# Optimization experiments

Hardware: AMD Instinct MI355X
Metric: run time of the kernel (lower is better)

## Reference

```python
import jax, jax.numpy as jnp
import numpy as np

EMBED_DIM = 1024
NUM_HEADS = 16
HEAD_DIM = EMBED_DIM // NUM_HEADS
NUM_GLOBAL = 2
NUM_RANDOM = 3
WINDOW_SIZE = 3
B, S = 2, 2048


def setup_inputs() -> dict:
    key = jax.random.key(0)
    ks = jax.random.split(key, 10)
    scale = 0.02
    inp = {
        "x": jax.random.normal(ks[0], (B, S, EMBED_DIM), dtype=jnp.float32),
        "random_indices": jax.random.randint(ks[1], (S, NUM_RANDOM), 0, S, dtype=jnp.int32),
        "q_w": jax.random.normal(ks[2], (EMBED_DIM, EMBED_DIM), dtype=jnp.float32) * scale,
        "q_b": jnp.zeros((EMBED_DIM,), dtype=jnp.float32),
        "k_w": jax.random.normal(ks[3], (EMBED_DIM, EMBED_DIM), dtype=jnp.float32) * scale,
        "k_b": jnp.zeros((EMBED_DIM,), dtype=jnp.float32),
        "v_w": jax.random.normal(ks[4], (EMBED_DIM, EMBED_DIM), dtype=jnp.float32) * scale,
        "v_b": jnp.zeros((EMBED_DIM,), dtype=jnp.float32),
        "o_w": jax.random.normal(ks[5], (EMBED_DIM, EMBED_DIM), dtype=jnp.float32) * scale,
        "o_b": jnp.zeros((EMBED_DIM,), dtype=jnp.float32),
    }
    return inp


def _build_mask(random_indices, seq_len):
    # [S, S] boolean BigBird mask: global rows/cols + sliding window + random.
    i = jnp.arange(seq_len)[:, None]
    j = jnp.arange(seq_len)[None, :]
    glob = (i < NUM_GLOBAL) | (j < NUM_GLOBAL)
    win = jnp.abs(i - j) <= WINDOW_SIZE
    rand = jnp.zeros((seq_len, seq_len), dtype=bool)
    rows = jnp.repeat(jnp.arange(seq_len), NUM_RANDOM)
    rand = rand.at[rows, random_indices.reshape(-1)].set(True)
    return glob | win | rand


def reference(x, random_indices, q_w, q_b, k_w, k_b, v_w, v_b, o_w, o_b):
    b, s, _ = x.shape
    # torch nn.Linear: y = x @ W.T + b
    q = (x @ q_w.T + q_b).reshape(b, s, NUM_HEADS, HEAD_DIM).transpose(0, 2, 1, 3)
    k = (x @ k_w.T + k_b).reshape(b, s, NUM_HEADS, HEAD_DIM).transpose(0, 2, 1, 3)
    v = (x @ v_w.T + v_b).reshape(b, s, NUM_HEADS, HEAD_DIM).transpose(0, 2, 1, 3)
    scores = jnp.einsum("bhqd,bhkd->bhqk", q, k) / jnp.sqrt(jnp.float32(HEAD_DIM))
    mask = _build_mask(random_indices, s)  # [S, S]
    scores = jnp.where(mask[None, None, :, :], scores, -jnp.inf)
    probs = jax.nn.softmax(scores, axis=-1)
    out = jnp.einsum("bhqk,bhkd->bhqd", probs, v)
    out = out.transpose(0, 2, 1, 3).reshape(b, s, EMBED_DIM)
    return out @ o_w.T + o_b
```

## Files before the change

kernel.cpp:

```cpp
#include <hip/hip_runtime.h>

#define B_  2
#define S_  2048
#define E_  1024
#define H_  16
#define D_  64
#define NGLOB 2
#define NRAND 3
#define WIN 3

typedef __bf16 bf16x8 __attribute__((ext_vector_type(8)));
typedef float  f32x4  __attribute__((ext_vector_type(4)));

__device__ __forceinline__ unsigned short f2bf(float f) {
    unsigned u = __builtin_bit_cast(unsigned, f);
    unsigned r = u + 0x7FFFu + ((u >> 16) & 1u);
    return (unsigned short)(r >> 16);
}
__device__ __forceinline__ float bf2f(unsigned short u) {
    return __builtin_bit_cast(float, (unsigned)u << 16);
}

__device__ __forceinline__ void g2l16(const unsigned short* g, unsigned short* l) {
    __builtin_amdgcn_global_load_lds(
        (const __attribute__((address_space(1))) unsigned*)g,
        (__attribute__((address_space(3))) unsigned*)l, 16, 0, 0);
}

__global__ __launch_bounds__(256)
void convert_all(const float* __restrict__ x,  const float* __restrict__ qw,
                 const float* __restrict__ kw, const float* __restrict__ vw,
                 const float* __restrict__ ow,
                 unsigned short* __restrict__ xb, unsigned short* __restrict__ wqkv,
                 unsigned short* __restrict__ wo) {
    const int XN = (B_ * S_ * E_) / 4;
    const int WN = (E_ * E_) / 4;
    int i = blockIdx.x * blockDim.x + threadIdx.x;
    int r, loc;
    if (i < XN) { r = 0; loc = i; }
    else        { int j = i - XN; r = 1 + (j >> 18); loc = j & (WN - 1); }
    const float* src = r == 0 ? x : r == 1 ? qw : r == 2 ? kw : r == 3 ? vw : ow;
    float4 f = ((const float4*)src)[loc];
    ushort4 u;
    u.x = f2bf(f.x); u.y = f2bf(f.y); u.z = f2bf(f.z); u.w = f2bf(f.w);
    ushort4* dst = r == 0 ? (ushort4*)xb : r == 4 ? (ushort4*)wo
                 : (ushort4*)wqkv + (size_t)(r - 1) * WN;
    dst[loc] = u;
}

__global__ __launch_bounds__(256, 3)
void gemm_qkv(const unsigned short* __restrict__ A,
              const unsigned short* __restrict__ W,
              const float* __restrict__ b0, const float* __restrict__ b1,
              const float* __restrict__ b2,
              unsigned short* __restrict__ Cb, int M, int N, int K) {
    __shared__ unsigned short sA[128 * 64];
    __shared__ unsigned short sB[128 * 64];
    const int t = threadIdx.x;
    const int lane = t & 63;
    const int wave = t >> 6;
    const int wm = wave >> 1, wn = wave & 1;
    const int lq = lane >> 4;
    const int lr = lane & 15;
    const int bm = blockIdx.x * 128;
    const int bn = blockIdx.y * 128;

    f32x4 acc[4][4] = {};

    for (int k0 = 0; k0 < K; k0 += 64) {
        const unsigned short* Abase = A + (size_t)bm * K + k0;
        const unsigned short* Wbase = W + (size_t)bn * K + k0;
        #pragma unroll
        for (int j = 0; j < 4; ++j) {
            int c = j * 256 + t;
            int row = c >> 3, cc = c & 7;
            int gcol = ((cc ^ (row & 7)) << 3);
            int dst = j * 2048 + wave * 512;
            g2l16(Abase + (size_t)row * K + gcol, sA + dst);
            g2l16(Wbase + (size_t)row * K + gcol, sB + dst);
        }
        __syncthreads();

        #pragma unroll
        for (int ks = 0; ks < 2; ++ks) {
            const int sw = (((ks << 2) + lq) ^ (lr & 7)) << 3;
            bf16x8 af[4], bfr[4];
            #pragma unroll
            for (int i = 0; i < 4; ++i)
                af[i] = *(const bf16x8*)&sA[(wm * 64 + i * 16 + lr) * 64 + sw];
            #pragma unroll
            for (int j = 0; j < 4; ++j)
                bfr[j] = *(const bf16x8*)&sB[(wn * 64 + j * 16 + lr) * 64 + sw];
            #pragma unroll
            for (int i = 0; i < 4; ++i)
                #pragma unroll
                for (int j = 0; j < 4; ++j)
                    acc[i][j] = __builtin_amdgcn_mfma_f32_16x16x32_bf16(af[i], bfr[j], acc[i][j], 0, 0, 0);
        }
        __syncthreads();
    }

    #pragma unroll
    for (int i = 0; i < 4; ++i) {
        int row0 = bm + wm * 64 + i * 16 + lq * 4;
        #pragma unroll
        for (int j = 0; j < 4; ++j) {
            int col = bn + wn * 64 + j * 16 + lr;
            const float* bp = col < E_ ? b0 : (col < 2 * E_ ? b1 : b2);
            float bv = bp[col & (E_ - 1)];
            #pragma unroll
            for (int r = 0; r < 4; ++r)
                Cb[(size_t)(row0 + r) * N + col] = f2bf(acc[i][j][r] + bv);
        }
    }
}

__global__ __launch_bounds__(256, 2)
void gemm_o64(const unsigned short* __restrict__ A,
              const unsigned short* __restrict__ W,
              const float* __restrict__ bias,
              float* __restrict__ Cf, int M, int N, int K) {
    __shared__ unsigned short sA[128 * 64];
    __shared__ unsigned short sB[64 * 64];
    const int t = threadIdx.x;
    const int lane = t & 63;
    const int wave = t >> 6;
    const int lq = lane >> 4;
    const int lr = lane & 15;
    const int bm = blockIdx.x * 128;
    const int bn = blockIdx.y * 64;

    f32x4 acc[2][4] = {};

    for (int k0 = 0; k0 < K; k0 += 64) {
        const unsigned short* Abase = A + (size_t)bm * K + k0;
        const unsigned short* Wbase = W + (size_t)bn * K + k0;
        #pragma unroll
        for (int j = 0; j < 4; ++j) {
            int c = j * 256 + t;
            int row = c >> 3, cc = c & 7;
            int gcol = ((cc ^ (row & 7)) << 3);
            int dst = j * 2048 + wave * 512;
            g2l16(Abase + (size_t)row * K + gcol, sA + dst);
        }
        #pragma unroll
        for (int j = 0; j < 2; ++j) {
            int c = j * 256 + t;
            int row = c >> 3, cc = c & 7;
            int gcol = ((cc ^ (row & 7)) << 3);
            int dst = j * 2048 + wave * 512;
            g2l16(Wbase + (size_t)row * K + gcol, sB + dst);
        }
        __syncthreads();

        #pragma unroll
        for (int ks = 0; ks < 2; ++ks) {
            const int sw = (((ks << 2) + lq) ^ (lr & 7)) << 3;
            bf16x8 af[2], bfr[4];
            #pragma unroll
            for (int i = 0; i < 2; ++i)
                af[i] = *(const bf16x8*)&sA[(wave * 32 + i * 16 + lr) * 64 + sw];
            #pragma unroll
            for (int j = 0; j < 4; ++j)
                bfr[j] = *(const bf16x8*)&sB[(j * 16 + lr) * 64 + sw];
            #pragma unroll
            for (int i = 0; i < 2; ++i)
                #pragma unroll
                for (int j = 0; j < 4; ++j)
                    acc[i][j] = __builtin_amdgcn_mfma_f32_16x16x32_bf16(af[i], bfr[j], acc[i][j], 0, 0, 0);
        }
        __syncthreads();
    }

    #pragma unroll
    for (int i = 0; i < 2; ++i) {
        int row0 = bm + wave * 32 + i * 16 + lq * 4;
        #pragma unroll
        for (int j = 0; j < 4; ++j) {
            int col = bn + j * 16 + lr;
            float bv = bias[col];
            #pragma unroll
            for (int r = 0; r < 4; ++r)
                Cf[(size_t)(row0 + r) * N + col] = acc[i][j][r] + bv;
        }
    }
}

__global__ __launch_bounds__(256)
void attn_fused(const unsigned short* __restrict__ qkv,
                const int* __restrict__ rnd,
                float* __restrict__ gaccp, float* __restrict__ gms,
                unsigned short* __restrict__ attn) {
    const int NB = B_ * (S_ - 2);
    int t = threadIdx.x;

    if (blockIdx.x < 512) {
        int tup = blockIdx.x >> 3, seg = blockIdx.x & 7;
        int b = tup >> 5, i = (tup >> 4) & 1, h = tup & 15;
        int w = t >> 6, l = t & 63;
        __shared__ float ps[256];
        __shared__ float red[4];
        __shared__ float ov[4][D_];

        const bf16x8* qp = (const bf16x8*)(qkv + (size_t)(b * S_ + i) * 3072 + h * D_);
        bf16x8 qv = qp[l & 7];
        float qreg[8];
        #pragma unroll
        for (int j = 0; j < 8; ++j) qreg[j] = (float)qv[j];

        const int key0 = seg * 256 + w * 64;
        float sc[8];
        #pragma unroll
        for (int it = 0; it < 8; ++it) {
            int key = key0 + it * 8 + (l >> 3);
            const bf16x8* kp = (const bf16x8*)(qkv + (size_t)(b * S_ + key) * 3072 + E_ + h * D_);
            bf16x8 kv = kp[l & 7];
            float s = 0.f;
            #pragma unroll
            for (int j = 0; j < 8; ++j) s += qreg[j] * (float)kv[j];
            s += __shfl_xor(s, 1);
            s += __shfl_xor(s, 2);
            s += __shfl_xor(s, 4);
            sc[it] = s * 0.125f;
        }
        #pragma unroll
        for (int it = 0; it < 8; ++it)
            if ((l & 7) == 0) ps[w * 64 + it * 8 + (l >> 3)] = sc[it];
        __syncthreads();

        float v = ps[t];
        float m = v;
        #pragma unroll
        for (int o = 32; o; o >>= 1) m = fmaxf(m, __shfl_xor(m, o));
        if (l == 0) red[w] = m;
        __syncthreads();
        m = fmaxf(fmaxf(red[0], red[1]), fmaxf(red[2], red[3]));
        float e = __expf(v - m);
        float sum = e;
        #pragma unroll
        for (int o = 32; o; o >>= 1) sum += __shfl_xor(sum, o);
        __syncthreads();
        if (l == 0) red[w] = sum;
        ps[t] = e;
        __syncthreads();
        if (t == 0) {
            float stot = red[0] + red[1] + red[2] + red[3];
            gms[(tup * 8 + seg) * 2]     = m;
            gms[(tup * 8 + seg) * 2 + 1] = stot;
        }

        const unsigned short* vbase =
            qkv + (size_t)(b * S_ + key0) * 3072 + 2 * E_ + h * D_ + l;
        const float* pw = ps + w * 64;
        float acc = 0.f;
        #pragma unroll 8
        for (int k = 0; k < 64; ++k)
            acc += pw[k] * bf2f(vbase[(size_t)k * 3072]);
        ov[w][l] = acc;
        __syncthreads();
        if (w == 0)
            gaccp[((size_t)tup * 8 + seg) * D_ + l] =
                ov[0][l] + ov[1][l] + ov[2][l] + ov[3][l];
        return;
    }

    int bb = blockIdx.x - 512;
    int bidx = (bb & 7) * 128 + (bb >> 3);
    int w = t >> 6, l = t & 63;
    int row = bidx * 4 + w;
    bool valid = row < NB;
    int b = row / (S_ - 2);
    int i = row % (S_ - 2) + 2;
    if (!valid) { b = 0; i = 2; }

    __shared__ int   cols_s[4][12];
    __shared__ int   ncol_sh[4];
    __shared__ float pr_s[4][16 * 13 + 3];

    const bf16x8* qp = (const bf16x8*)(qkv + (size_t)(b * S_ + i) * 3072);
    bf16x8 q0 = qp[l * 2], q1 = qp[l * 2 + 1];
    float qreg[16];
    #pragma unroll
    for (int j = 0; j < 8; ++j) { qreg[j] = (float)q0[j]; qreg[8 + j] = (float)q1[j]; }

    if (l == 0) {
        int* cols = cols_s[w];
        int n = 0;
        cols[n++] = 0; cols[n++] = 1;
        int lo = i - WIN; if (lo < NGLOB) lo = NGLOB;
        int hi = i + WIN; if (hi > S_ - 1) hi = S_ - 1;
        for (int j = lo; j <= hi; ++j) cols[n++] = j;
        for (int r = 0; r < NRAND; ++r) {
            int c = rnd[i * NRAND + r];
            bool dup = false;
            for (int q = 0; q < n; ++q) dup = dup || (cols[q] == c);
            if (!dup) cols[n++] = c;
        }
        ncol_sh[w] = n;
        for (int q = n; q < 12; ++q) cols[q] = 0;
    }
    __syncthreads();
    const int n = ncol_sh[w];
    const int h4 = l >> 2;

    float sco[12];
    #pragma unroll
    for (int c = 0; c < 12; ++c) {
        const bf16x8* kp = (const bf16x8*)(qkv + (size_t)(b * S_ + cols_s[w][c]) * 3072 + E_);
        bf16x8 k0 = kp[l * 2], k1 = kp[l * 2 + 1];
        float s = 0.f;
        #pragma unroll
        for (int j = 0; j < 8; ++j) s += qreg[j] * (float)k0[j] + qreg[8 + j] * (float)k1[j];
        s += __shfl_xor(s, 1);
        s += __shfl_xor(s, 2);
        sco[c] = (c < n) ? s * 0.125f : -1e30f;
    }

    if ((l & 3) == 0) {
        float m = -1e30f;
        #pragma unroll
        for (int c = 0; c < 12; ++c) m = fmaxf(m, sco[c]);
        float sum = 0.f;
        #pragma unroll
        for (int c = 0; c < 12; ++c) { float e = __expf(sco[c] - m); sco[c] = e; sum += e; }
        float inv = 1.f / sum;
        #pragma unroll
        for (int c = 0; c < 12; ++c) pr_s[w][h4 * 13 + c] = sco[c] * inv;
    }
    __syncthreads();

    float o[16] = {};
    #pragma unroll
    for (int c = 0; c < 12; ++c) {
        float p = pr_s[w][h4 * 13 + c];
        const bf16x8* vp = (const bf16x8*)(qkv + (size_t)(b * S_ + cols_s[w][c]) * 3072 + 2 * E_);
        bf16x8 v0 = vp[l * 2], v1 = vp[l * 2 + 1];
        #pragma unroll
        for (int j = 0; j < 8; ++j) { o[j] += p * (float)v0[j]; o[8 + j] += p * (float)v1[j]; }
    }

    if (valid) {
        ushort4 u0, u1, u2, u3;
        u0.x = f2bf(o[0]);  u0.y = f2bf(o[1]);  u0.z = f2bf(o[2]);  u0.w = f2bf(o[3]);
        u1.x = f2bf(o[4]);  u1.y = f2bf(o[5]);  u1.z = f2bf(o[6]);  u1.w = f2bf(o[7]);
        u2.x = f2bf(o[8]);  u2.y = f2bf(o[9]);  u2.z = f2bf(o[10]); u2.w = f2bf(o[11]);
        u3.x = f2bf(o[12]); u3.y = f2bf(o[13]); u3.z = f2bf(o[14]); u3.w = f2bf(o[15]);
        ushort4* op = (ushort4*)(attn + (size_t)(b * S_ + i) * E_ + l * 16);
        op[0] = u0; op[1] = u1; op[2] = u2; op[3] = u3;
    }
}

__global__ __launch_bounds__(256)
void gattn_fin(const float* __restrict__ gaccp, const float* __restrict__ gms,
               unsigned short* __restrict__ attn) {
    int gid = blockIdx.x * 256 + threadIdx.x;
    int tup = gid >> 6, d = gid & 63;
    int b = tup >> 5, i = (tup >> 4) & 1, h = tup & 15;
    float mc[8], sc[8], M = -1e30f;
    #pragma unroll
    for (int c = 0; c < 8; ++c) {
        mc[c] = gms[(tup * 8 + c) * 2];
        sc[c] = gms[(tup * 8 + c) * 2 + 1];
        M = fmaxf(M, mc[c]);
    }
    float den = 0.f, num = 0.f;
    #pragma unroll
    for (int c = 0; c < 8; ++c) {
        float f = __expf(mc[c] - M);
        den += sc[c] * f;
        num += gaccp[((size_t)tup * 8 + c) * D_ + d] * f;
    }
    attn[(size_t)(b * S_ + i) * E_ + h * D_ + d] = f2bf(num / den);
}

extern "C" void kernel_launch(void* const* d_in, const int* in_sizes, int n_in,
                              void* d_out, int out_size, void* d_ws, size_t ws_size,
                              hipStream_t stream) {
    const float* x   = (const float*)d_in[0];
    const int*   rnd = (const int*)d_in[1];
    const float* qw  = (const float*)d_in[2];
    const float* qb  = (const float*)d_in[3];
    const float* kw  = (const float*)d_in[4];
    const float* kb  = (const float*)d_in[5];
    const float* vw  = (const float*)d_in[6];
    const float* vb  = (const float*)d_in[7];
    const float* ow  = (const float*)d_in[8];
    const float* ob  = (const float*)d_in[9];
    float* out = (float*)d_out;

    char* ws = (char*)d_ws;
    unsigned short* xb    = (unsigned short*)(ws);
    unsigned short* wqkv  = (unsigned short*)(ws + 8388608);
    unsigned short* wo    = (unsigned short*)(ws + 14680064);
    unsigned short* qkv   = (unsigned short*)(ws + 16777216);
    unsigned short* attn  = (unsigned short*)(ws + 41943040);
    float*          gaccp = (float*)(ws);
    float*          gms   = (float*)(ws + 131072);

    const int M = B_ * S_;

    {
        int total4 = (M * E_ + 4 * E_ * E_) / 4;
        convert_all<<<total4 / 256, 256, 0, stream>>>(x, qw, kw, vw, ow, xb, wqkv, wo);
    }

    {
        dim3 grid(M / 128, 3 * E_ / 128);
        gemm_qkv<<<grid, 256, 0, stream>>>(xb, wqkv, qb, kb, vb, qkv, M, 3 * E_, E_);
    }

    attn_fused<<<512 + 1024, 256, 0, stream>>>(qkv, rnd, gaccp, gms, attn);

    gattn_fin<<<16, 256, 0, stream>>>(gaccp, gms, attn);

    {
        dim3 grid(M / 128, E_ / 64);
        gemm_o64<<<grid, 256, 0, stream>>>(attn, wo, ob, out, M, E_, E_);
    }
}
```

Before: 167.3 us.

## Remap GEMM workgroups across XCDs and enlarge output-projection tiles to 128x128

Both GEMMs now use a 1D grid whose workgroup ids are remapped so consecutive ids land on the same XCD. Each XCD then works on a contiguous band of tiles, which is meant to improve L2 reuse of the A and W panels. The output projection also moves from 128x64 tiles to 128x128 tiles laid out as 2x2 waves, raising per-wave MFMA work and reuse. That halves its grid to 256 workgroups, which may hurt occupancy and tail balance on the 256-CU device.

```diff
diff --git a/kernel.cpp b/kernel.cpp
--- a/kernel.cpp
+++ b/kernel.cpp
@@ -56,14 +56,16 @@
               unsigned short* __restrict__ Cb, int M, int N, int K) {
     __shared__ unsigned short sA[128 * 64];
     __shared__ unsigned short sB[128 * 64];
+    const int nwg = gridDim.x;
+    const int id  = (blockIdx.x & 7) * (nwg >> 3) + (blockIdx.x >> 3);
+    const int bm = (id & 31) * 128;
+    const int bn = (id >> 5) * 128;
     const int t = threadIdx.x;
     const int lane = t & 63;
     const int wave = t >> 6;
     const int wm = wave >> 1, wn = wave & 1;
     const int lq = lane >> 4;
     const int lr = lane & 15;
-    const int bm = blockIdx.x * 128;
-    const int bn = blockIdx.y * 128;
 
     f32x4 acc[4][4] = {};
 
@@ -115,22 +117,25 @@
     }
 }
 
-__global__ __launch_bounds__(256, 2)
-void gemm_o64(const unsigned short* __restrict__ A,
-              const unsigned short* __restrict__ W,
-              const float* __restrict__ bias,
-              float* __restrict__ Cf, int M, int N, int K) {
+__global__ __launch_bounds__(256, 3)
+void gemm_o(const unsigned short* __restrict__ A,
+            const unsigned short* __restrict__ W,
+            const float* __restrict__ bias,
+            float* __restrict__ Cf, int M, int N, int K) {
     __shared__ unsigned short sA[128 * 64];
-    __shared__ unsigned short sB[64 * 64];
+    __shared__ unsigned short sB[128 * 64];
+    const int nwg = gridDim.x;
+    const int id  = (blockIdx.x & 7) * (nwg >> 3) + (blockIdx.x >> 3);
+    const int bm = (id & 31) * 128;
+    const int bn = (id >> 5) * 128;
     const int t = threadIdx.x;
     const int lane = t & 63;
     const int wave = t >> 6;
+    const int wm = wave >> 1, wn = wave & 1;
     const int lq = lane >> 4;
     const int lr = lane & 15;
-    const int bm = blockIdx.x * 128;
-    const int bn = blockIdx.y * 64;
-
-    f32x4 acc[2][4] = {};
+
+    f32x4 acc[4][4] = {};
 
     for (int k0 = 0; k0 < K; k0 += 64) {
         const unsigned short* Abase = A + (size_t)bm * K + k0;
@@ -142,13 +147,6 @@
             int gcol = ((cc ^ (row & 7)) << 3);
             int dst = j * 2048 + wave * 512;
             g2l16(Abase + (size_t)row * K + gcol, sA + dst);
-        }
-        #pragma unroll
-        for (int j = 0; j < 2; ++j) {
-            int c = j * 256 + t;
-            int row = c >> 3, cc = c & 7;
-            int gcol = ((cc ^ (row & 7)) << 3);
-            int dst = j * 2048 + wave * 512;
             g2l16(Wbase + (size_t)row * K + gcol, sB + dst);
         }
         __syncthreads();
@@ -156,15 +154,15 @@
         #pragma unroll
         for (int ks = 0; ks < 2; ++ks) {
             const int sw = (((ks << 2) + lq) ^ (lr & 7)) << 3;
-            bf16x8 af[2], bfr[4];
-            #pragma unroll
-            for (int i = 0; i < 2; ++i)
-                af[i] = *(const bf16x8*)&sA[(wave * 32 + i * 16 + lr) * 64 + sw];
+            bf16x8 af[4], bfr[4];
+            #pragma unroll
+            for (int i = 0; i < 4; ++i)
+                af[i] = *(const bf16x8*)&sA[(wm * 64 + i * 16 + lr) * 64 + sw];
             #pragma unroll
             for (int j = 0; j < 4; ++j)
-                bfr[j] = *(const bf16x8*)&sB[(j * 16 + lr) * 64 + sw];
-            #pragma unroll
-            for (int i = 0; i < 2; ++i)
+                bfr[j] = *(const bf16x8*)&sB[(wn * 64 + j * 16 + lr) * 64 + sw];
+            #pragma unroll
+            for (int i = 0; i < 4; ++i)
                 #pragma unroll
                 for (int j = 0; j < 4; ++j)
                     acc[i][j] = __builtin_amdgcn_mfma_f32_16x16x32_bf16(af[i], bfr[j], acc[i][j], 0, 0, 0);
@@ -173,11 +171,11 @@
     }
 
     #pragma unroll
-    for (int i = 0; i < 2; ++i) {
-        int row0 = bm + wave * 32 + i * 16 + lq * 4;
+    for (int i = 0; i < 4; ++i) {
+        int row0 = bm + wm * 64 + i * 16 + lq * 4;
         #pragma unroll
         for (int j = 0; j < 4; ++j) {
-            int col = bn + j * 16 + lr;
+            int col = bn + wn * 64 + j * 16 + lr;
             float bv = bias[col];
             #pragma unroll
             for (int r = 0; r < 4; ++r)
@@ -404,17 +402,11 @@
         convert_all<<<total4 / 256, 256, 0, stream>>>(x, qw, kw, vw, ow, xb, wqkv, wo);
     }
 
-    {
-        dim3 grid(M / 128, 3 * E_ / 128);
-        gemm_qkv<<<grid, 256, 0, stream>>>(xb, wqkv, qb, kb, vb, qkv, M, 3 * E_, E_);
-    }
+    gemm_qkv<<<768, 256, 0, stream>>>(xb, wqkv, qb, kb, vb, qkv, M, 3 * E_, E_);
 
     attn_fused<<<512 + 1024, 256, 0, stream>>>(qkv, rnd, gaccp, gms, attn);
 
     gattn_fin<<<16, 256, 0, stream>>>(gaccp, gms, attn);
 
-    {
-        dim3 grid(M / 128, E_ / 64);
-        gemm_o64<<<grid, 256, 0, stream>>>(attn, wo, ob, out, M, E_, E_);
-    }
-}
+    gemm_o<<<256, 256, 0, stream>>>(attn, wo, ob, out, M, E_, E_);
+}
```

Result: no change. 169.7 us (+1.4%).
